# Kernel tuning notes

Hardware: AMD Instinct MI355X
Metric: run time of the kernel (lower is better)

## Reference

```python
import jax, jax.numpy as jnp
import numpy as np

N = 100_000          # nodes
E_RAND = 1_600_000   # random edges (avg degree 16)
IN, H, F, SEQ = 64, 4, 16, 10
FLAT = H * F * SEQ   # 640, MLP input width
MLP_DIMS = [FLAT, 180, 150, 128, 80, 64, 32, 1]


def setup_inputs() -> dict:
    key = jax.random.key(0)
    ks = jax.random.split(key, 32)
    x = jax.random.normal(ks[0], (N, IN), jnp.float32)
    # edges + self loops (dgl.add_self_loop)
    src = jnp.concatenate([jax.random.randint(ks[1], (E_RAND,), 0, N), jnp.arange(N)]).astype(jnp.int32)
    dst = jnp.concatenate([jax.random.randint(ks[2], (E_RAND,), 0, N), jnp.arange(N)]).astype(jnp.int32)
    inp = {"x": x, "src": src, "dst": dst}
    # GATConv params (fc has no bias in DGL; bias added post-aggregation)
    inp["fc_w"] = (jax.random.normal(ks[3], (IN, H * F), jnp.float32) / np.sqrt(IN).astype(np.float32))
    inp["bias"] = jnp.zeros((H * F,), jnp.float32)
    inp["attn_l"] = jax.random.normal(ks[4], (H, F), jnp.float32) * 0.1
    inp["attn_r"] = jax.random.normal(ks[5], (H, F), jnp.float32) * 0.1
    # deep MLP params
    for i in range(7):
        di, do = MLP_DIMS[i], MLP_DIMS[i + 1]
        inp[f"w{i+1}"] = jax.random.normal(ks[6 + i], (di, do), jnp.float32) / np.sqrt(di).astype(np.float32)
        inp[f"b{i+1}"] = jnp.zeros((do,), jnp.float32)
    inp["wt"] = jax.random.normal(ks[20], (FLAT, 1), jnp.float32) / np.sqrt(FLAT).astype(np.float32)
    return inp


def reference(x, src, dst, fc_w, bias, attn_l, attn_r,
              w1, b1, w2, b2, w3, b3, w4, b4, w5, b5, w6, b6, w7, b7, wt):
    # --- GATConv ---
    feat = (x @ fc_w).reshape(N, H, F)                      # [N,H,F]
    el = jnp.einsum('nhf,hf->nh', feat, attn_l)             # [N,H]
    er = jnp.einsum('nhf,hf->nh', feat, attn_r)
    e = jax.nn.leaky_relu(el[src] + er[dst], 0.2)           # [E,H]
    # edge softmax over incoming edges of each dst node
    m = jax.ops.segment_max(e, dst, num_segments=N)         # [N,H]
    ez = jnp.exp(e - m[dst])
    denom = jax.ops.segment_sum(ez, dst, num_segments=N)
    alpha = ez / denom[dst]                                 # [E,H]
    msg = alpha[:, :, None] * feat[src]                     # [E,H,F]
    out = jax.ops.segment_sum(msg, dst, num_segments=N) + bias.reshape(1, H, F)
    # --- flatten SEQ nodes per path, deep MLP + linear_trans ---
    g = out.reshape(N // SEQ, FLAT)                         # [P,640]
    h = g
    layers = [(w1, b1), (w2, b2), (w3, b3), (w4, b4), (w5, b5), (w6, b6), (w7, b7)]
    for i, (w, b) in enumerate(layers):
        h = h @ w + b
        if i < len(layers) - 1:
            h = jax.nn.relu(h)
    wx = g @ wt                                             # [P,1]
    return h + wx
```

## Files before the change

kernel.cpp:

```cpp
#include <hip/hip_runtime.h>
#include <hip/hip_bf16.h>
#include <hip/hip_fp16.h>

#define N_NODES 100000
#define P_PATHS 10000
#define NBUK 391
#define FEAT_BLKS 782
#define HIST_BLKS 416
#define WPREP_BLKS 94

typedef __attribute__((ext_vector_type(8))) short s16x8;
typedef __attribute__((ext_vector_type(4))) short s16x4;
typedef __attribute__((ext_vector_type(4))) float f32x4;
typedef __attribute__((ext_vector_type(8))) _Float16 f16x8;

__device__ __forceinline__ short f2bf(float v) {
    return __builtin_bit_cast(short, __float2bfloat16(v));
}
__device__ __forceinline__ float bf2f(short s) {
    return __bfloat162float(__builtin_bit_cast(__hip_bfloat16, s));
}
__device__ __forceinline__ float h2f(short s) {
    return __half2float(__builtin_bit_cast(__half, s));
}
__device__ __forceinline__ short f2h(float v) {
    return __builtin_bit_cast(short, __float2half(v));
}

__global__ __launch_bounds__(256) void k_fused1(const float* __restrict__ x,
                                                const float* __restrict__ fc_w,
                                                const float* __restrict__ attn_l,
                                                const float* __restrict__ attn_r,
                                                __half* __restrict__ feat,
                                                float* __restrict__ el,
                                                float* __restrict__ er,
                                                const int* __restrict__ dst,
                                                int* __restrict__ buktot,
                                                const float* __restrict__ w1,
                                                const float* __restrict__ w2,
                                                const float* __restrict__ w3,
                                                const float* __restrict__ w4,
                                                const float* __restrict__ w5,
                                                const float* __restrict__ w6,
                                                short* __restrict__ wf, int E) {
    __shared__ float s_w[64 * 64];
    __shared__ float s_wx[64 * 16];
    __shared__ int hcnt[NBUK];
    int tid = threadIdx.x;
    int bb = blockIdx.x;

    if (bb < FEAT_BLKS) {
        for (int i = tid; i < 4096; i += 256) s_w[i] = fc_w[i];
        __syncthreads();
        for (int i = tid; i < 1024; i += 256) {
            int k = i >> 4, c = i & 15;
            float v = 0.f;
            if (c < 8) {
                int h = c & 3;
                const float* av = (c < 4) ? attn_l : attn_r;
                for (int f = 0; f < 16; ++f) v += s_w[k * 64 + h * 16 + f] * av[h * 16 + f];
            }
            s_wx[i] = v;
        }
        __syncthreads();

        int w = tid >> 6, l = tid & 63;
        int c_lane = l & 15, kg = l >> 4;

        s16x8 wh[5][2], wlo[5][2];
#pragma unroll
        for (int ct = 0; ct < 5; ++ct)
#pragma unroll
            for (int ks = 0; ks < 2; ++ks) {
                s16x8 h8, l8;
#pragma unroll
                for (int i = 0; i < 8; ++i) {
                    int k = ks * 32 + kg * 8 + i;
                    float v = (ct < 4) ? s_w[k * 64 + ct * 16 + c_lane]
                                       : s_wx[k * 16 + c_lane];
                    short hi = f2bf(v);
                    h8[i] = hi;
                    l8[i] = f2bf(v - bf2f(hi));
                }
                wh[ct][ks] = h8;
                wlo[ct][ks] = l8;
            }

        int nbase = bb * 128 + w * 32;
#pragma unroll 1
        for (int mt = 0; mt < 2; ++mt) {
            int m0 = nbase + mt * 16;
            if (m0 >= N_NODES) break;
            int arow = m0 + c_lane;
            size_t axoff = (size_t)(arow < N_NODES ? arow : N_NODES - 1) * 64;
            s16x8 ah[2], alo[2];
#pragma unroll
            for (int ks = 0; ks < 2; ++ks) {
                const float* xp = x + axoff + ks * 32 + kg * 8;
                float4 v0 = *(const float4*)xp;
                float4 v1 = *(const float4*)(xp + 4);
                float vv[8] = {v0.x, v0.y, v0.z, v0.w, v1.x, v1.y, v1.z, v1.w};
                s16x8 h8, l8;
#pragma unroll
                for (int i = 0; i < 8; ++i) {
                    short hi = f2bf(vv[i]);
                    h8[i] = hi;
                    l8[i] = f2bf(vv[i] - bf2f(hi));
                }
                ah[ks] = h8;
                alo[ks] = l8;
            }
            int r0 = m0 + kg * 4;
#pragma unroll
            for (int ct = 0; ct < 5; ++ct) {
                f32x4 acc = {0.f, 0.f, 0.f, 0.f};
#pragma unroll
                for (int ks = 0; ks < 2; ++ks) {
                    acc = __builtin_amdgcn_mfma_f32_16x16x32_bf16(ah[ks], wh[ct][ks], acc, 0, 0, 0);
                    acc = __builtin_amdgcn_mfma_f32_16x16x32_bf16(ah[ks], wlo[ct][ks], acc, 0, 0, 0);
                    acc = __builtin_amdgcn_mfma_f32_16x16x32_bf16(alo[ks], wh[ct][ks], acc, 0, 0, 0);
                }
                if (ct < 4) {
#pragma unroll
                    for (int j = 0; j < 4; ++j) {
                        int r = r0 + j;
                        if (r < N_NODES)
                            feat[(size_t)r * 64 + ct * 16 + c_lane] = __float2half(acc[j]);
                    }
                } else {
                    if (c_lane < 4) {
#pragma unroll
                        for (int j = 0; j < 4; ++j) {
                            int r = r0 + j;
                            if (r < N_NODES) el[r * 4 + c_lane] = acc[j];
                        }
                    } else if (c_lane < 8) {
#pragma unroll
                        for (int j = 0; j < 4; ++j) {
                            int r = r0 + j;
                            if (r < N_NODES) er[r * 4 + (c_lane - 4)] = acc[j];
                        }
                    }
                }
            }
        }
    } else if (bb < FEAT_BLKS + HIST_BLKS) {
        int hb = bb - FEAT_BLKS;
        for (int i = tid; i < NBUK; i += 256) hcnt[i] = 0;
        __syncthreads();
#pragma unroll
        for (int j = 0; j < 4; ++j) {
            int i = hb * 4096 + j * 1024 + tid * 4;
            if (i + 3 < E) {
                int4 d4 = *(const int4*)(dst + i);
                atomicAdd(&hcnt[d4.x >> 8], 1);
                atomicAdd(&hcnt[d4.y >> 8], 1);
                atomicAdd(&hcnt[d4.z >> 8], 1);
                atomicAdd(&hcnt[d4.w >> 8], 1);
            } else {
                for (int k = i; k < E && k < i + 4; ++k)
                    atomicAdd(&hcnt[dst[k] >> 8], 1);
            }
        }
        __syncthreads();
        for (int i = tid; i < NBUK; i += 256)
            if (hcnt[i]) atomicAdd(buktot + i, hcnt[i]);
    } else {
        const int nblk[6] = {240, 60, 40, 20, 12, 4};
        const int din_[6] = {640, 180, 150, 128, 80, 64};
        const int dout_[6] = {180, 150, 128, 80, 64, 32};
        const int ks_[6]  = {20, 6, 5, 4, 3, 2};
        const int off_[6] = {0, 122880, 153600, 174080, 184320, 190464};
        const float* wp[6] = {w1, w2, w3, w4, w5, w6};

        int b = (bb - FEAT_BLKS - HIST_BLKS) * 4 + (tid >> 6);
        int layer = 0;
        while (layer < 5 && b >= nblk[layer]) { b -= nblk[layer]; ++layer; }
        int KS = ks_[layer];
        int ct = b / KS, ks = b % KS;
        int l = tid & 63;
        int c = ct * 16 + (l & 15);
        int k0 = ks * 32 + ((l >> 4) * 8);
        int din = din_[layer], dout = dout_[layer];
        const float* w = wp[layer];
        s16x8 vh;
#pragma unroll
        for (int i = 0; i < 8; ++i) {
            int k = k0 + i;
            float v = (k < din && c < dout) ? w[k * dout + c] : 0.f;
            vh[i] = f2h(v);
        }
        size_t o = (size_t)off_[layer] + ((size_t)(ct * KS + ks) * 64 + l) * 8;
        *(s16x8*)(wf + o) = vh;
    }
}

__global__ __launch_bounds__(512) void k_scanB(const int* __restrict__ buktot,
                                               int* __restrict__ bukstart,
                                               int* __restrict__ bukptr,
                                               int* __restrict__ rowptr, int E) {
    __shared__ int s[512];
    int tid = threadIdx.x;
    int v = (tid < NBUK) ? buktot[tid] : 0;
    s[tid] = v;
    __syncthreads();
    for (int off = 1; off < 512; off <<= 1) {
        int t = (tid >= off) ? s[tid - off] : 0;
        __syncthreads();
        s[tid] += t;
        __syncthreads();
    }
    int excl = s[tid] - v;
    if (tid < NBUK) { bukstart[tid] = excl; bukptr[tid] = excl; }
    if (tid == 0) { bukstart[NBUK] = E; rowptr[N_NODES] = E; }
}

__global__ __launch_bounds__(256) void k_bucketA(const int* __restrict__ src,
                                                 const int* __restrict__ dst,
                                                 int* __restrict__ bukptr,
                                                 unsigned* __restrict__ pair, int E) {
    __shared__ int cnt[NBUK];
    __shared__ int base[NBUK];
    int tid = threadIdx.x;
    for (int i = tid; i < NBUK; i += 256) cnt[i] = 0;
    __syncthreads();
    int b0 = blockIdx.x * 2048;
    int s[8], d[8], off[8];
#pragma unroll
    for (int j = 0; j < 8; ++j) {
        int i = b0 + j * 256 + tid;
        if (i < E) {
            s[j] = src[i];
            d[j] = dst[i];
            off[j] = atomicAdd(&cnt[d[j] >> 8], 1);
        } else {
            d[j] = -1; s[j] = 0; off[j] = 0;
        }
    }
    __syncthreads();
    for (int i = tid; i < NBUK; i += 256)
        base[i] = cnt[i] ? atomicAdd(bukptr + i, cnt[i]) : 0;
    __syncthreads();
#pragma unroll
    for (int j = 0; j < 8; ++j) {
        if (d[j] >= 0) {
            int pos = base[d[j] >> 8] + off[j];
            pair[pos] = (unsigned)s[j] | ((unsigned)(d[j] & 255) << 17);
        }
    }
}

__global__ __launch_bounds__(256) void k_bucketC(const unsigned* __restrict__ pair,
                                                 const int* __restrict__ bukstart,
                                                 int* __restrict__ rowptr,
                                                 int* __restrict__ csr, int E) {
    __shared__ int cnt[256];
    __shared__ int s[256];
    __shared__ int wofs[256];
    int buk = blockIdx.x, tid = threadIdx.x;
    int p0 = bukstart[buk], p1 = bukstart[buk + 1];
    cnt[tid] = 0;
    __syncthreads();
    for (int i = p0 + tid; i < p1; i += 256)
        atomicAdd(&cnt[pair[i] >> 17], 1);
    __syncthreads();
    int v = cnt[tid];
    s[tid] = v;
    __syncthreads();
    for (int off = 1; off < 256; off <<= 1) {
        int t = (tid >= off) ? s[tid - off] : 0;
        __syncthreads();
        s[tid] += t;
        __syncthreads();
    }
    int r = p0 + s[tid] - v;
    wofs[tid] = r;
    int node = (buk << 8) + tid;
    if (node < N_NODES) rowptr[node] = r;
    __syncthreads();
    for (int i = p0 + tid; i < p1; i += 256) {
        unsigned p = pair[i];
        int pos = atomicAdd(&wofs[p >> 17], 1);
        csr[pos] = (int)(p & 0x1FFFFu);
    }
}

__global__ __launch_bounds__(256) void k_agg(const int* __restrict__ rowptr,
                                             const int* __restrict__ csr,
                                             const float* __restrict__ el,
                                             const float* __restrict__ er,
                                             const __half* __restrict__ feat,
                                             const float* __restrict__ bias,
                                             __half* __restrict__ agg) {
    int tid = threadIdx.x;
    int wave = tid >> 6, lane = tid & 63;
    int slot = lane >> 3;
    int fl = lane & 7;
    int n = blockIdx.x * 4 + wave;
    if (n >= N_NODES) return;
    int h = fl >> 1;
    float ern = er[(size_t)n * 4 + h];
    int e0 = rowptr[n], e1 = rowptr[n + 1];
    f32x4 a0 = {0.f,0.f,0.f,0.f}, b0 = {0.f,0.f,0.f,0.f};
    f32x4 a1 = {0.f,0.f,0.f,0.f}, b1 = {0.f,0.f,0.f,0.f};
    float den0 = 0.f, den1 = 0.f;
    int e = e0 + slot;
    for (; e + 8 < e1; e += 16) {
        int s0 = csr[e], s1 = csr[e + 8];
        s16x8 v0 = *(const s16x8*)(feat + (size_t)s0 * 64 + fl * 8);
        s16x8 v1 = *(const s16x8*)(feat + (size_t)s1 * 64 + fl * 8);
        float ev0 = el[(size_t)s0 * 4 + h] + ern;
        float ev1 = el[(size_t)s1 * 4 + h] + ern;
        ev0 = ev0 > 0.f ? ev0 : 0.2f * ev0;
        ev1 = ev1 > 0.f ? ev1 : 0.2f * ev1;
        float ez0 = __expf(ev0);
        float ez1 = __expf(ev1);
#pragma unroll
        for (int t = 0; t < 4; ++t) {
            a0[t] += ez0 * h2f(v0[t]);
            b0[t] += ez0 * h2f(v0[t + 4]);
            a1[t] += ez1 * h2f(v1[t]);
            b1[t] += ez1 * h2f(v1[t + 4]);
        }
        den0 += ez0;
        den1 += ez1;
    }
    for (; e < e1; e += 8) {
        int s0 = csr[e];
        s16x8 v0 = *(const s16x8*)(feat + (size_t)s0 * 64 + fl * 8);
        float ev0 = el[(size_t)s0 * 4 + h] + ern;
        ev0 = ev0 > 0.f ? ev0 : 0.2f * ev0;
        float ez0 = __expf(ev0);
#pragma unroll
        for (int t = 0; t < 4; ++t) {
            a0[t] += ez0 * h2f(v0[t]);
            b0[t] += ez0 * h2f(v0[t + 4]);
        }
        den0 += ez0;
    }
    float den = den0 + den1;
    f32x4 a, b;
#pragma unroll
    for (int t = 0; t < 4; ++t) { a[t] = a0[t] + a1[t]; b[t] = b0[t] + b1[t]; }
#pragma unroll
    for (int t = 0; t < 4; ++t) {
        a[t] += __shfl_xor(a[t], 32);
        a[t] += __shfl_xor(a[t], 16);
        a[t] += __shfl_xor(a[t], 8);
        b[t] += __shfl_xor(b[t], 32);
        b[t] += __shfl_xor(b[t], 16);
        b[t] += __shfl_xor(b[t], 8);
    }
    den += __shfl_xor(den, 32);
    den += __shfl_xor(den, 16);
    den += __shfl_xor(den, 8);
    if (slot == 0) {
        float inv = 1.f / den;
        s16x8 o;
#pragma unroll
        for (int t = 0; t < 4; ++t) {
            o[t]     = f2h(a[t] * inv + bias[fl * 8 + t]);
            o[t + 4] = f2h(b[t] * inv + bias[fl * 8 + t + 4]);
        }
        *(s16x8*)(agg + (size_t)n * 64 + fl * 8) = o;
    }
}

template <int KS, int CT>
__device__ __forceinline__ void mfma_layer16(const short* sa, int sstride,
                                             short* dst_,
                                             const short* __restrict__ wf,
                                             const float* __restrict__ bias,
                                             int dout, int w, int l) {
    int abase = (l & 15) * sstride + ((l >> 4) * 8);
    int c_lane = l & 15;
    for (int ct = w; ct < CT; ct += 4) {
        f32x4 acc = {0.f, 0.f, 0.f, 0.f};
        const f16x8* wp = (const f16x8*)wf + (size_t)(ct * KS) * 64 + l;
#pragma unroll
        for (int ks = 0; ks < KS; ++ks) {
            f16x8 av = *(const f16x8*)(sa + abase + ks * 32);
            f16x8 wv = wp[ks * 64];
            acc = __builtin_amdgcn_mfma_f32_16x16x32_f16(av, wv, acc, 0, 0, 0);
        }
        int c = ct * 16 + c_lane;
        float bb = (c < dout) ? bias[c] : 0.f;
        int row0 = (l >> 4) * 4;
#pragma unroll
        for (int j = 0; j < 4; ++j) {
            float v = acc[j] + bb;
            v = v > 0.f ? v : 0.f;
            dst_[(row0 + j) * 200 + c] = f2h(v);
        }
    }
}

__global__ __launch_bounds__(256) void k_mlp(const __half* __restrict__ agg,
                                             const short* __restrict__ wf,
                                             const float* __restrict__ b1,
                                             const float* __restrict__ b2,
                                             const float* __restrict__ b3,
                                             const float* __restrict__ b4,
                                             const float* __restrict__ b5,
                                             const float* __restrict__ b6,
                                             const float* __restrict__ w7,
                                             const float* __restrict__ b7,
                                             const float* __restrict__ wt,
                                             float* __restrict__ outp) {
    __shared__ __align__(16) short smem[13600];
    __shared__ float wx[16];
    short* g  = smem;
    short* h0 = smem + 10368;
    short* h1 = smem;

    int tid = threadIdx.x;
    int w = tid >> 6, l = tid & 63;
    int p0 = blockIdx.x * 16;

    const s16x8* a8 = (const s16x8*)(agg + (size_t)p0 * 640);
    for (int i = tid; i < 16 * 80; i += 256) {
        int r = i / 80, c8 = (i % 80) * 8;
        *(s16x8*)(g + r * 648 + c8) = a8[i];
    }

    if (tid < 128) {
        int path = tid >> 3, sub = tid & 7;
        const __half* gr = agg + (size_t)(p0 + path) * 640;
        float acc = 0.f;
        for (int k = sub * 4; k < 640; k += 32) {
            s16x4 gv = *(const s16x4*)(gr + k);
            float4 wv = *(const float4*)(wt + k);
            acc += h2f(gv[0]) * wv.x + h2f(gv[1]) * wv.y
                 + h2f(gv[2]) * wv.z + h2f(gv[3]) * wv.w;
        }
        acc += __shfl_xor(acc, 1);
        acc += __shfl_xor(acc, 2);
        acc += __shfl_xor(acc, 4);
        if (sub == 0) wx[path] = acc;
    }
    __syncthreads();

    mfma_layer16<20, 12>(g, 648, h0, wf + 0,      b1, 180, w, l);
    __syncthreads();
    mfma_layer16<6, 10>(h0, 200, h1, wf + 122880, b2, 150, w, l);
    __syncthreads();
    mfma_layer16<5, 8>(h1, 200, h0, wf + 153600, b3, 128, w, l);
    __syncthreads();
    mfma_layer16<4, 5>(h0, 200, h1, wf + 174080, b4, 80, w, l);
    {
        int r = tid >> 4, c = 80 + (tid & 15);
        h1[r * 200 + c] = 0;
    }
    __syncthreads();
    mfma_layer16<3, 4>(h1, 200, h0, wf + 184320, b5, 64, w, l);
    __syncthreads();
    mfma_layer16<2, 2>(h0, 200, h1, wf + 190464, b6, 32, w, l);
    __syncthreads();

    if (tid < 16) {
        float acc = b7[0];
#pragma unroll
        for (int k = 0; k < 32; ++k)
            acc += h2f(h1[tid * 200 + k]) * w7[k];
        outp[p0 + tid] = acc + wx[tid];
    }
}

extern "C" void kernel_launch(void* const* d_in, const int* in_sizes, int n_in,
                              void* d_out, int out_size, void* d_ws, size_t ws_size,
                              hipStream_t stream) {
    const float* x      = (const float*)d_in[0];
    const int*   src    = (const int*)d_in[1];
    const int*   dst    = (const int*)d_in[2];
    const float* fc_w   = (const float*)d_in[3];
    const float* bias   = (const float*)d_in[4];
    const float* attn_l = (const float*)d_in[5];
    const float* attn_r = (const float*)d_in[6];
    const float* w1 = (const float*)d_in[7];  const float* b1 = (const float*)d_in[8];
    const float* w2 = (const float*)d_in[9];  const float* b2 = (const float*)d_in[10];
    const float* w3 = (const float*)d_in[11]; const float* b3 = (const float*)d_in[12];
    const float* w4 = (const float*)d_in[13]; const float* b4 = (const float*)d_in[14];
    const float* w5 = (const float*)d_in[15]; const float* b5 = (const float*)d_in[16];
    const float* w6 = (const float*)d_in[17]; const float* b6 = (const float*)d_in[18];
    const float* w7 = (const float*)d_in[19]; const float* b7 = (const float*)d_in[20];
    const float* wt = (const float*)d_in[21];
    int E = in_sizes[1];

    float* ws      = (float*)d_ws;
    __half* feat   = (__half*)ws;
    float* el      = ws + 6400000;
    float* er      = ws + 6800000;
    __half* agg    = (__half*)(ws + 7200000);
    unsigned* pair = (unsigned*)(ws + 10400000);
    int*   rowptr  = (int*)(ws + 13600000);
    int*   buktot  = (int*)(ws + 13700004);
    int*   bukstart= (int*)(ws + 13700400);
    int*   bukptr  = (int*)(ws + 13700800);
    int*   csr     = (int*)(ws + 13701200);
    short* wf      = (short*)(ws + 13701200 + E);

    int nwgA = (E + 2047) / 2048;

    hipMemsetAsync(buktot, 0, NBUK * 4, stream);

    k_fused1<<<FEAT_BLKS + HIST_BLKS + WPREP_BLKS, 256, 0, stream>>>(
        x, fc_w, attn_l, attn_r, feat, el, er, dst, buktot,
        w1, w2, w3, w4, w5, w6, wf, E);
    k_scanB<<<1, 512, 0, stream>>>(buktot, bukstart, bukptr, rowptr, E);
    k_bucketA<<<nwgA, 256, 0, stream>>>(src, dst, bukptr, pair, E);
    k_bucketC<<<NBUK, 256, 0, stream>>>(pair, bukstart, rowptr, csr, E);
    k_agg<<<N_NODES / 4, 256, 0, stream>>>(rowptr, csr, el, er, feat, bias, agg);
    k_mlp<<<P_PATHS / 16, 256, 0, stream>>>(agg, wf, b1, b2, b3, b4, b5, b6,
                                            w7, b7, wt, (float*)d_out);
}
```

Baseline: 159.1 us.

## Stage bucket scatter in LDS, swizzle agg blocks, fold log2e into el/er

The bucketing kernel now sorts each block's 2048 edge pairs by bucket in shared memory using a local prefix scan. It then writes them to global memory in sorted order, so stores to each bucket are contiguous rather than scattered per thread. The aggregation kernel remaps block IDs with an XCD-style swizzle (blocks with the same id mod 8 get contiguous node ranges), intended to improve L2 locality across chiplets. The attention projection weights are pre-scaled by log2(e) so exp2f can replace __expf; this is valid because leaky_relu is positively homogeneous. The cost is extra LDS usage and an added scan in the bucket kernel.

New measurement: 156.1 us. About the same (-1.9%).

```diff
diff --git a/kernel.cpp b/kernel.cpp
--- a/kernel.cpp
+++ b/kernel.cpp
@@ -8,6 +8,7 @@
 #define FEAT_BLKS 782
 #define HIST_BLKS 416
 #define WPREP_BLKS 94
+#define LOG2E 1.4426950408889634f
 
 typedef __attribute__((ext_vector_type(8))) short s16x8;
 typedef __attribute__((ext_vector_type(4))) short s16x4;
@@ -60,7 +61,7 @@
                 const float* av = (c < 4) ? attn_l : attn_r;
                 for (int f = 0; f < 16; ++f) v += s_w[k * 64 + h * 16 + f] * av[h * 16 + f];
             }
-            s_wx[i] = v;
+            s_wx[i] = v * LOG2E;
         }
         __syncthreads();
 
@@ -220,34 +221,59 @@
                                                  int* __restrict__ bukptr,
                                                  unsigned* __restrict__ pair, int E) {
     __shared__ int cnt[NBUK];
-    __shared__ int base[NBUK];
+    __shared__ int seg[NBUK];
+    __shared__ int gbase[NBUK];
+    __shared__ unsigned sbuf[2048];
+    __shared__ int gaddr[2048];
+    __shared__ int csum[256];
     int tid = threadIdx.x;
     for (int i = tid; i < NBUK; i += 256) cnt[i] = 0;
     __syncthreads();
     int b0 = blockIdx.x * 2048;
-    int s[8], d[8], off[8];
+    int sv[8], dv[8], off[8];
 #pragma unroll
     for (int j = 0; j < 8; ++j) {
         int i = b0 + j * 256 + tid;
         if (i < E) {
-            s[j] = src[i];
-            d[j] = dst[i];
-            off[j] = atomicAdd(&cnt[d[j] >> 8], 1);
+            sv[j] = src[i];
+            dv[j] = dst[i];
+            off[j] = atomicAdd(&cnt[dv[j] >> 8], 1);
         } else {
-            d[j] = -1; s[j] = 0; off[j] = 0;
-        }
-    }
+            dv[j] = -1; sv[j] = 0; off[j] = 0;
+        }
+    }
+    __syncthreads();
+    int c0 = (2 * tid < NBUK) ? cnt[2 * tid] : 0;
+    int c1 = (2 * tid + 1 < NBUK) ? cnt[2 * tid + 1] : 0;
+    int psum = c0 + c1;
+    csum[tid] = psum;
+    __syncthreads();
+    for (int o2 = 1; o2 < 256; o2 <<= 1) {
+        int t = (tid >= o2) ? csum[tid - o2] : 0;
+        __syncthreads();
+        csum[tid] += t;
+        __syncthreads();
+    }
+    int pexcl = csum[tid] - psum;
+    if (2 * tid < NBUK) seg[2 * tid] = pexcl;
+    if (2 * tid + 1 < NBUK) seg[2 * tid + 1] = pexcl + c0;
     __syncthreads();
     for (int i = tid; i < NBUK; i += 256)
-        base[i] = cnt[i] ? atomicAdd(bukptr + i, cnt[i]) : 0;
+        gbase[i] = cnt[i] ? atomicAdd(bukptr + i, cnt[i]) : 0;
     __syncthreads();
 #pragma unroll
     for (int j = 0; j < 8; ++j) {
-        if (d[j] >= 0) {
-            int pos = base[d[j] >> 8] + off[j];
-            pair[pos] = (unsigned)s[j] | ((unsigned)(d[j] & 255) << 17);
-        }
-    }
+        if (dv[j] >= 0) {
+            int b = dv[j] >> 8;
+            int k = seg[b] + off[j];
+            sbuf[k] = (unsigned)sv[j] | ((unsigned)(dv[j] & 255) << 17);
+            gaddr[k] = gbase[b] + off[j];
+        }
+    }
+    __syncthreads();
+    int tot = E - b0; if (tot > 2048) tot = 2048;
+    for (int k = tid; k < tot; k += 256)
+        pair[gaddr[k]] = sbuf[k];
 }
 
 __global__ __launch_bounds__(256) void k_bucketC(const unsigned* __restrict__ pair,
@@ -296,7 +322,9 @@
     int wave = tid >> 6, lane = tid & 63;
     int slot = lane >> 3;
     int fl = lane & 7;
-    int n = blockIdx.x * 4 + wave;
+    int bid = blockIdx.x;
+    int swz = (bid & 7) * 3125 + (bid >> 3);
+    int n = swz * 4 + wave;
     if (n >= N_NODES) return;
     int h = fl >> 1;
     float ern = er[(size_t)n * 4 + h];
@@ -313,8 +341,8 @@
         float ev1 = el[(size_t)s1 * 4 + h] + ern;
         ev0 = ev0 > 0.f ? ev0 : 0.2f * ev0;
         ev1 = ev1 > 0.f ? ev1 : 0.2f * ev1;
-        float ez0 = __expf(ev0);
-        float ez1 = __expf(ev1);
+        float ez0 = exp2f(ev0);
+        float ez1 = exp2f(ev1);
 #pragma unroll
         for (int t = 0; t < 4; ++t) {
             a0[t] += ez0 * h2f(v0[t]);
@@ -330,7 +358,7 @@
         s16x8 v0 = *(const s16x8*)(feat + (size_t)s0 * 64 + fl * 8);
         float ev0 = el[(size_t)s0 * 4 + h] + ern;
         ev0 = ev0 > 0.f ? ev0 : 0.2f * ev0;
-        float ez0 = __expf(ev0);
+        float ez0 = exp2f(ev0);
 #pragma unroll
         for (int t = 0; t < 4; ++t) {
             a0[t] += ez0 * h2f(v0[t]);
```
